# Optimization experiments

Measured on AMD Instinct MI355X. Metric: run time of the kernel, lower is better.

The kernel has to match this reference:

```python
import jax, jax.numpy as jnp
import numpy as np

K = 3
PAD = 1
EPS = 1e-5


def _conv2d(x, w, b):
    y = jax.lax.conv_general_dilated(x, w, window_strides=(1, 1), padding='SAME',
                                     dimension_numbers=('NCHW', 'OIHW', 'NCHW'))
    return y + b[None, :, None, None]


def _bn(x, g, beta, m, v):
    inv = jax.lax.rsqrt(v + EPS)
    return (x - m[None, :, None, None]) * (g * inv)[None, :, None, None] + beta[None, :, None, None]


def _deform_conv2d(x, offset, w, b):
    # torchvision deform_conv2d (v1, no mask), stride=1, pad=1, 3x3 kernel.
    B, Cin, H, W = x.shape
    Cout = w.shape[0]
    # offset: [B, 2*K*K, H, W] -> (dy, dx) per kernel tap
    off = offset.reshape(B, K * K, 2, H, W)
    dy, dx = off[:, :, 0], off[:, :, 1]                     # [B, K2, H, W]
    ii, jj = jnp.meshgrid(jnp.arange(K), jnp.arange(K), indexing='ij')
    ki = (ii.reshape(-1) - PAD).astype(x.dtype)             # [K2]
    kj = (jj.reshape(-1) - PAD).astype(x.dtype)
    py = jnp.arange(H, dtype=x.dtype)[None, None, :, None] + ki[None, :, None, None] + dy
    px = jnp.arange(W, dtype=x.dtype)[None, None, None, :] + kj[None, :, None, None] + dx
    y0 = jnp.floor(py)
    x0 = jnp.floor(px)
    wy = py - y0
    wx = px - x0
    flat = x.reshape(B, Cin, H * W)

    def gather(yc, xc):
        valid = ((yc >= 0) & (yc < H) & (xc >= 0) & (xc < W)).astype(x.dtype)
        yi = jnp.clip(yc, 0, H - 1).astype(jnp.int32)
        xi = jnp.clip(xc, 0, W - 1).astype(jnp.int32)
        idx = (yi * W + xi).reshape(B, -1)                  # [B, K2*H*W]
        g = jax.vmap(lambda f, i: f[:, i])(flat, idx)       # [B, Cin, K2*H*W]
        return g.reshape(B, Cin, K * K, H, W) * valid[:, None]

    v = (gather(y0,     x0    ) * ((1 - wy) * (1 - wx))[:, None]
         + gather(y0,     x0 + 1) * ((1 - wy) * wx)[:, None]
         + gather(y0 + 1, x0    ) * (wy * (1 - wx))[:, None]
         + gather(y0 + 1, x0 + 1) * (wy * wx)[:, None])     # [B, Cin, K2, H, W]
    out = jnp.einsum('bckhw,ock->bohw', v, w.reshape(Cout, Cin, K * K))
    return out + b[None, :, None, None]


def setup_inputs() -> dict:
    key = jax.random.key(0)
    ks = jax.random.split(key, 12)
    d = {}
    d['x'] = jax.random.normal(ks[0], (32, 3, 64, 64), jnp.float32)
    d['offset1_w'] = jax.random.normal(ks[1], (18, 3, 3, 3), jnp.float32) * 0.05
    d['offset1_b'] = jnp.zeros((18,), jnp.float32)
    d['conv1_w'] = jax.random.normal(ks[2], (64, 3, 3, 3), jnp.float32) * 0.1
    d['conv1_b'] = jnp.zeros((64,), jnp.float32)
    d['bn1_gamma'] = jnp.ones((64,), jnp.float32)
    d['bn1_beta'] = jnp.zeros((64,), jnp.float32)
    d['bn1_mean'] = jnp.zeros((64,), jnp.float32)
    d['bn1_var'] = jax.random.uniform(ks[3], (64,), jnp.float32, 0.5, 1.5)
    d['offset2_w'] = jax.random.normal(ks[4], (18, 64, 3, 3), jnp.float32) * 0.02
    d['offset2_b'] = jnp.zeros((18,), jnp.float32)
    d['conv2_w'] = jax.random.normal(ks[5], (128, 64, 3, 3), jnp.float32) * 0.05
    d['conv2_b'] = jnp.zeros((128,), jnp.float32)
    d['bn2_gamma'] = jnp.ones((128,), jnp.float32)
    d['bn2_beta'] = jnp.zeros((128,), jnp.float32)
    d['bn2_mean'] = jnp.zeros((128,), jnp.float32)
    d['bn2_var'] = jax.random.uniform(ks[6], (128,), jnp.float32, 0.5, 1.5)
    d['fc1_w'] = jax.random.normal(ks[7], (256, 128), jnp.float32) * 0.08
    d['fc1_b'] = jnp.zeros((256,), jnp.float32)
    d['fc2_w'] = jax.random.normal(ks[8], (200, 256), jnp.float32) * 0.06
    d['fc2_b'] = jnp.zeros((200,), jnp.float32)
    return d


def reference(x, offset1_w, offset1_b, conv1_w, conv1_b, bn1_gamma, bn1_beta, bn1_mean, bn1_var,
              offset2_w, offset2_b, conv2_w, conv2_b, bn2_gamma, bn2_beta, bn2_mean, bn2_var,
              fc1_w, fc1_b, fc2_w, fc2_b):
    # Eval-mode forward (dropout layers are identity / deterministic).
    off1 = _conv2d(x, offset1_w, offset1_b)
    h = _deform_conv2d(x, off1, conv1_w, conv1_b)
    h = jax.nn.relu(_bn(h, bn1_gamma, bn1_beta, bn1_mean, bn1_var))
    off2 = _conv2d(h, offset2_w, offset2_b)
    h = _deform_conv2d(h, off2, conv2_w, conv2_b)
    h = jax.nn.relu(_bn(h, bn2_gamma, bn2_beta, bn2_mean, bn2_var))
    h = h.mean(axis=(2, 3))                                 # global avg pool -> [B, 128]
    h = jax.nn.relu(h @ fc1_w.T + fc1_b)
    return h @ fc2_w.T + fc2_b
```

## Files before the change

### kernel.cpp

```cpp
#include <hip/hip_runtime.h>

#define EPS 1e-5f

#define W1OT 0
#define W1T  1024
#define W2T  4096
#define W2OB 40960
#define SC1  59392
#define SH1  59456
#define SC2  59520
#define SH2  59648
#define POOL 59776
#define XP   65536
#define H1B  589824
#define OFF2 4784128
#define W2T_U   8192
#define W2OB_U  81920
#define H1B_U   1179648

typedef __attribute__((ext_vector_type(8))) short bhalf8;
typedef __attribute__((ext_vector_type(8))) unsigned short u16x8;
typedef __attribute__((ext_vector_type(4))) float f32x4;

#define BPAD 72
#define OPAD 584

struct Tap { int i00, i01, i10, i11; float w00, w01, w10, w11; };

__device__ __forceinline__ Tap make_tap(float py, float px) {
    float y0f = floorf(py), x0f = floorf(px);
    float wy = py - y0f, wx = px - x0f;
    bool by0 = (y0f >= 0.f)  && (y0f < 64.f);
    bool by1 = (y0f >= -1.f) && (y0f < 63.f);
    bool bx0 = (x0f >= 0.f)  && (x0f < 64.f);
    bool bx1 = (x0f >= -1.f) && (x0f < 63.f);
    int y0 = min(max((int)y0f, 0), 63);
    int y1 = min(max((int)y0f + 1, 0), 63);
    int x0 = min(max((int)x0f, 0), 63);
    int x1 = min(max((int)x0f + 1, 0), 63);
    Tap tp;
    tp.i00 = y0 * 64 + x0; tp.i01 = y0 * 64 + x1;
    tp.i10 = y1 * 64 + x0; tp.i11 = y1 * 64 + x1;
    tp.w00 = (by0 && bx0) ? (1.f - wy) * (1.f - wx) : 0.f;
    tp.w01 = (by0 && bx1) ? (1.f - wy) * wx         : 0.f;
    tp.w10 = (by1 && bx0) ? wy * (1.f - wx)         : 0.f;
    tp.w11 = (by1 && bx1) ? wy * wx                 : 0.f;
    return tp;
}

__device__ __forceinline__ ushort f2bf(float f) {
    union { float f; uint u; } a; a.f = f;
    uint u = a.u;
    return (ushort)((u + 0x7fffu + ((u >> 16) & 1u)) >> 16);
}
__device__ __forceinline__ float bf2f(ushort u) {
    union { uint u; float f; } a; a.u = ((uint)u) << 16;
    return a.f;
}

__global__ __launch_bounds__(256) void k_prep(
    const float* __restrict__ x,
    const float* __restrict__ o1w, const float* __restrict__ c1w,
    const float* __restrict__ o2w, const float* __restrict__ c2w,
    const float* __restrict__ c1b, const float* __restrict__ g1,
    const float* __restrict__ be1, const float* __restrict__ m1,
    const float* __restrict__ v1,
    const float* __restrict__ c2b, const float* __restrict__ g2,
    const float* __restrict__ be2, const float* __restrict__ m2,
    const float* __restrict__ v2,
    float* __restrict__ ws) {
    int tid = blockIdx.x * 256 + threadIdx.x;
    ushort* wsu = (ushort*)ws;
    if (tid < 648) {
        int co = tid % 18, tc = tid / 18, c = tc & 3, t = tc >> 2;
        ws[W1OT + tid] = (c < 3) ? o1w[(co * 3 + c) * 9 + t] : 0.f;
    } else if (tid < 2952) {
        int i = tid - 648;
        int co = i & 63, tc = i >> 6, c = tc & 3, t = tc >> 2;
        ws[W1T + i] = (c < 3) ? c1w[(co * 3 + c) * 9 + t] : 0.f;
    } else if (tid < 76680) {
        int i = tid - 2952;
        int c = i & 63, n = (i >> 6) & 127, t = i >> 13;
        wsu[W2T_U + i] = f2bf(c2w[(n * 64 + c) * 9 + t]);
    } else if (tid < 95112) {
        int i = tid - 76680;
        int n = i / 576, k = i - n * 576;
        int c = k & 63, t = k >> 6;
        float v = (n < 18) ? o2w[(n * 64 + c) * 9 + t] : 0.f;
        wsu[W2OB_U + i] = f2bf(v);
    } else if (tid < 95176) {
        int i = tid - 95112;
        float s = g1[i] * rsqrtf(v1[i] + EPS);
        ws[SC1 + i] = s;
        ws[SH1 + i] = (c1b[i] - m1[i]) * s + be1[i];
    } else if (tid < 95304) {
        int i = tid - 95176;
        float s = g2[i] * rsqrtf(v2[i] + EPS);
        ws[SC2 + i] = s;
        ws[SH2 + i] = (c2b[i] - m2[i]) * s + be2[i];
    } else if (tid < 99400) {
        ws[POOL + tid - 95304] = 0.f;
    } else if (tid < 230472) {
        int i = tid - 99400;
        int b = i >> 12, hw = i & 4095;
        const float* xpp = x + (size_t)b * 3 * 4096 + hw;
        f32x4 o;
        o[0] = xpp[0]; o[1] = xpp[4096]; o[2] = xpp[8192]; o[3] = 0.f;
        *(f32x4*)(ws + XP + (size_t)i * 4) = o;
    }
}

__global__ __launch_bounds__(256, 3) void k_def1(
    const float* __restrict__ o1b, float* __restrict__ ws) {
    __shared__ float wo[648];
    __shared__ float wt[2304];
    for (int i = threadIdx.x; i < 648; i += 256) wo[i] = ws[W1OT + i];
    for (int i = threadIdx.x; i < 2304; i += 256) wt[i] = ws[W1T + i];
    __syncthreads();
    int tid = blockIdx.x * 256 + threadIdx.x;
    int b = tid >> 12, hw = tid & 4095, h = hw >> 6, w = hw & 63;
    const float* xp = ws + XP + (size_t)b * 16384;
    float off[18];
#pragma unroll
    for (int i = 0; i < 18; ++i) off[i] = o1b[i];
#pragma unroll
    for (int t = 0; t < 9; ++t) {
        int yy = h + t / 3 - 1, xx = w + t % 3 - 1;
        f32x4 pv = (f32x4)0.f;
        if (yy >= 0 && yy < 64 && xx >= 0 && xx < 64)
            pv = *(const f32x4*)(xp + (yy * 64 + xx) * 4);
#pragma unroll
        for (int c = 0; c < 3; ++c) {
            const float* wp = wo + (t * 4 + c) * 18;
#pragma unroll
            for (int co = 0; co < 18; ++co) off[co] += pv[c] * wp[co];
        }
    }
    f32x4 v[9];
#pragma unroll
    for (int t = 0; t < 9; ++t) {
        Tap tp = make_tap((float)(h + t / 3 - 1) + off[2 * t],
                          (float)(w + t % 3 - 1) + off[2 * t + 1]);
        f32x4 c00 = *(const f32x4*)(xp + tp.i00 * 4);
        f32x4 c01 = *(const f32x4*)(xp + tp.i01 * 4);
        f32x4 c10 = *(const f32x4*)(xp + tp.i10 * 4);
        f32x4 c11 = *(const f32x4*)(xp + tp.i11 * 4);
        v[t] = tp.w00 * c00 + tp.w01 * c01 + tp.w10 * c10 + tp.w11 * c11;
    }
    const float* sc = ws + SC1;
    const float* sh = ws + SH1;
    ushort* op = (ushort*)ws + H1B_U + (size_t)(b * 4096 + hw) * 64;
#pragma unroll
    for (int ch = 0; ch < 2; ++ch) {
        float acc[32];
#pragma unroll
        for (int i = 0; i < 32; ++i) acc[i] = 0.f;
#pragma unroll
        for (int t = 0; t < 9; ++t)
#pragma unroll
            for (int c = 0; c < 3; ++c) {
                float vk = v[t][c];
                const float* wp = wt + (t * 4 + c) * 64 + ch * 32;
#pragma unroll
                for (int co = 0; co < 32; ++co) acc[co] += vk * wp[co];
            }
        ushort ob[32];
#pragma unroll
        for (int i = 0; i < 32; ++i) {
            int co = ch * 32 + i;
            ob[i] = f2bf(fmaxf(acc[i] * sc[co] + sh[co], 0.f));
        }
#pragma unroll
        for (int i = 0; i < 4; ++i)
            *(uint4*)(op + ch * 32 + i * 8) = *(const uint4*)(ob + i * 8);
    }
}

__global__ __launch_bounds__(256, 4) void k_off2(
    const float* __restrict__ o2b, float* __restrict__ ws) {
    __shared__ ushort Bl[32 * OPAD];
    int g = blockIdx.x;
    int b = (g & 7) * 4 + ((g >> 3) & 3);
    int row = g >> 5;
    int tid = threadIdx.x, lane = tid & 63, wv = tid >> 6;
    int r = lane & 15, q = lane >> 4;
    int hw0 = row * 64 + wv * 16;
    const ushort* hb = (const ushort*)ws + H1B_U + (size_t)b * 262144;
    const ushort* bt = (const ushort*)ws + W2OB_U;
    for (int i = tid; i < 2304; i += 256) {
        int n = i / 72, kk = (i - n * 72) * 8;
        *(uint4*)(Bl + n * OPAD + kk) = *(const uint4*)(bt + n * 576 + kk);
    }
    __syncthreads();
    f32x4 acc[2];
    acc[0] = (f32x4)0.f; acc[1] = (f32x4)0.f;
#pragma unroll
    for (int t = 0; t < 9; ++t) {
        int yy = row + t / 3 - 1;
        int xx = wv * 16 + r + t % 3 - 1;
        bool val = (yy >= 0 && yy < 64 && xx >= 0 && xx < 64);
        int yyc = min(max(yy, 0), 63), xxc = min(max(xx, 0), 63);
        const ushort* ap = hb + (size_t)(yyc * 64 + xxc) * 64 + q * 8;
#pragma unroll
        for (int ks = 0; ks < 2; ++ks) {
            bhalf8 af = val ? *(const bhalf8*)(ap + ks * 32) : (bhalf8)(short)0;
            int kk = t * 64 + ks * 32 + q * 8;
#pragma unroll
            for (int nt = 0; nt < 2; ++nt) {
                bhalf8 bf = *(const bhalf8*)(Bl + (nt * 16 + r) * OPAD + kk);
                acc[nt] = __builtin_amdgcn_mfma_f32_16x16x32_bf16(af, bf, acc[nt], 0, 0, 0);
            }
        }
    }
#pragma unroll
    for (int nt = 0; nt < 2; ++nt) {
        int n = nt * 16 + r;
        if (n < 18) {
            float bias = o2b[n];
#pragma unroll
            for (int rr = 0; rr < 4; ++rr) {
                int hw = hw0 + q * 4 + rr;
                ws[OFF2 + (size_t)(b * 4096 + hw) * 18 + n] = acc[nt][rr] + bias;
            }
        }
    }
}

__global__ __launch_bounds__(256, 5) void k_def2(float* __restrict__ ws) {
    __shared__ ushort Blds[128 * BPAD];
    int g = blockIdx.x;
    int b = (g & 7) * 4 + ((g >> 3) & 3);
    int row = g >> 5;
    int tid = threadIdx.x, lane = tid & 63, wv = tid >> 6;
    int r = lane & 15, q = lane >> 4;
    int px = wv * 16 + r;
    const ushort* hb = (const ushort*)ws + H1B_U + (size_t)b * 262144;
    const float* o2 = ws + OFF2 + (size_t)b * 73728 + (size_t)(row * 64 + px) * 18;
    const ushort* wB = (const ushort*)ws + W2T_U;
    int bn = tid >> 1, bc = (tid & 1) * 32;

    float2 off[9];
#pragma unroll
    for (int t = 0; t < 9; ++t) off[t] = *(const float2*)(o2 + 2 * t);

    f32x4 acc[8];
#pragma unroll
    for (int j = 0; j < 8; ++j) acc[j] = (f32x4)0.f;

    for (int t = 0; t < 9; ++t) {
        Tap tp = make_tap((float)(row + t / 3 - 1) + off[t].x,
                          (float)(px + t % 3 - 1) + off[t].y);
        if (t) __syncthreads();
        {
            const uint4* s4 = (const uint4*)(wB + (t * 128 + bn) * 64 + bc);
            uint4 p0 = s4[0], p1 = s4[1], p2 = s4[2], p3 = s4[3];
            ushort* dst = Blds + bn * BPAD + bc;
            *(uint4*)(dst)      = p0;
            *(uint4*)(dst + 8)  = p1;
            *(uint4*)(dst + 16) = p2;
            *(uint4*)(dst + 24) = p3;
        }
        __syncthreads();
#pragma unroll
        for (int ks = 0; ks < 2; ++ks) {
            int ko = ks * 32 + q * 8;
            bhalf8 bf[8];
#pragma unroll
            for (int nt = 0; nt < 8; ++nt)
                bf[nt] = *(const bhalf8*)(Blds + (nt * 16 + r) * BPAD + ko);
            u16x8 g00 = *(const u16x8*)(hb + (size_t)tp.i00 * 64 + ko);
            u16x8 g01 = *(const u16x8*)(hb + (size_t)tp.i01 * 64 + ko);
            u16x8 g10 = *(const u16x8*)(hb + (size_t)tp.i10 * 64 + ko);
            u16x8 g11 = *(const u16x8*)(hb + (size_t)tp.i11 * 64 + ko);
            f32x4 lo = (f32x4)0.f, hi = (f32x4)0.f;
#pragma unroll
            for (int j = 0; j < 4; ++j) {
                lo[j] = tp.w00 * bf2f(g00[j]) + tp.w01 * bf2f(g01[j])
                      + tp.w10 * bf2f(g10[j]) + tp.w11 * bf2f(g11[j]);
                hi[j] = tp.w00 * bf2f(g00[j + 4]) + tp.w01 * bf2f(g01[j + 4])
                      + tp.w10 * bf2f(g10[j + 4]) + tp.w11 * bf2f(g11[j + 4]);
            }
            bhalf8 af;
#pragma unroll
            for (int j = 0; j < 4; ++j) {
                af[j]     = (short)f2bf(lo[j]);
                af[j + 4] = (short)f2bf(hi[j]);
            }
#pragma unroll
            for (int nt = 0; nt < 8; ++nt)
                acc[nt] = __builtin_amdgcn_mfma_f32_16x16x32_bf16(af, bf[nt], acc[nt], 0, 0, 0);
        }
    }
    const float* sc = ws + SC2;
    const float* sh = ws + SH2;
    float* pool = ws + POOL;
#pragma unroll
    for (int nt = 0; nt < 8; ++nt) {
        int col = nt * 16 + r;
        float s0 = sc[col], s1 = sh[col];
        float s = 0.f;
#pragma unroll
        for (int rr = 0; rr < 4; ++rr)
            s += fmaxf(acc[nt][rr] * s0 + s1, 0.f);
        s += __shfl_xor(s, 16);
        s += __shfl_xor(s, 32);
        if (lane < 16) atomicAdd(&pool[b * 128 + col], s);
    }
}

__global__ __launch_bounds__(256) void k_fc(
    const float* __restrict__ w1, const float* __restrict__ b1,
    const float* __restrict__ w2, const float* __restrict__ b2,
    const float* __restrict__ ws, float* __restrict__ out) {
    int b = blockIdx.x, o = threadIdx.x;
    __shared__ float pl[128];
    __shared__ float hl[256];
    if (o < 128) pl[o] = ws[POOL + b * 128 + o] * (1.f / 4096.f);
    __syncthreads();
    float s = b1[o];
    const float* wp = w1 + o * 128;
#pragma unroll 8
    for (int c = 0; c < 128; ++c) s += pl[c] * wp[c];
    hl[o] = fmaxf(s, 0.f);
    __syncthreads();
    if (o < 200) {
        float s2 = b2[o];
        const float* wp2 = w2 + o * 256;
#pragma unroll 8
        for (int c = 0; c < 256; ++c) s2 += hl[c] * wp2[c];
        out[b * 200 + o] = s2;
    }
}

extern "C" void kernel_launch(void* const* d_in, const int* in_sizes, int n_in,
                              void* d_out, int out_size, void* d_ws, size_t ws_size,
                              hipStream_t stream) {
    const float* x   = (const float*)d_in[0];
    const float* o1w = (const float*)d_in[1];
    const float* o1b = (const float*)d_in[2];
    const float* c1w = (const float*)d_in[3];
    const float* c1b = (const float*)d_in[4];
    const float* g1  = (const float*)d_in[5];
    const float* be1 = (const float*)d_in[6];
    const float* m1  = (const float*)d_in[7];
    const float* v1  = (const float*)d_in[8];
    const float* o2w = (const float*)d_in[9];
    const float* o2b = (const float*)d_in[10];
    const float* c2w = (const float*)d_in[11];
    const float* c2b = (const float*)d_in[12];
    const float* g2  = (const float*)d_in[13];
    const float* be2 = (const float*)d_in[14];
    const float* m2  = (const float*)d_in[15];
    const float* v2  = (const float*)d_in[16];
    const float* f1w = (const float*)d_in[17];
    const float* f1b = (const float*)d_in[18];
    const float* f2w = (const float*)d_in[19];
    const float* f2b = (const float*)d_in[20];
    float* ws  = (float*)d_ws;
    float* out = (float*)d_out;

    k_prep<<<901, 256, 0, stream>>>(x, o1w, c1w, o2w, c2w,
                                    c1b, g1, be1, m1, v1,
                                    c2b, g2, be2, m2, v2, ws);
    k_def1<<<512, 256, 0, stream>>>(o1b, ws);
    k_off2<<<2048, 256, 0, stream>>>(o2b, ws);
    k_def2<<<2048, 256, 0, stream>>>(ws);
    k_fc<<<32, 256, 0, stream>>>(f1w, f1b, f2w, f2b, ws, out);
}
```

Measured before the change: 319.7 us.

## Fuse offset conv into deformable conv2 kernel via shared-memory offsets

Merges the offset-2 convolution kernel into the second deformable-conv kernel. Each block first computes its row's 18 offset channels with MFMA, stages them in LDS, and then runs the deformable sampling and GEMM in the same block. This removes one kernel launch and the global write and read of the offset tensor. In exchange the fused kernel uses more LDS and registers, and its launch bounds drop from 5 to 4 blocks per CU, so occupancy is lower.

```diff
diff --git a/kernel.cpp b/kernel.cpp
--- a/kernel.cpp
+++ b/kernel.cpp
@@ -13,7 +13,6 @@
 #define POOL 59776
 #define XP   65536
 #define H1B  589824
-#define OFF2 4784128
 #define W2T_U   8192
 #define W2OB_U  81920
 #define H1B_U   1179648
@@ -176,58 +175,11 @@
     }
 }
 
-__global__ __launch_bounds__(256, 4) void k_off2(
+__global__ __launch_bounds__(256, 4) void k_def2(
     const float* __restrict__ o2b, float* __restrict__ ws) {
-    __shared__ ushort Bl[32 * OPAD];
-    int g = blockIdx.x;
-    int b = (g & 7) * 4 + ((g >> 3) & 3);
-    int row = g >> 5;
-    int tid = threadIdx.x, lane = tid & 63, wv = tid >> 6;
-    int r = lane & 15, q = lane >> 4;
-    int hw0 = row * 64 + wv * 16;
-    const ushort* hb = (const ushort*)ws + H1B_U + (size_t)b * 262144;
-    const ushort* bt = (const ushort*)ws + W2OB_U;
-    for (int i = tid; i < 2304; i += 256) {
-        int n = i / 72, kk = (i - n * 72) * 8;
-        *(uint4*)(Bl + n * OPAD + kk) = *(const uint4*)(bt + n * 576 + kk);
-    }
-    __syncthreads();
-    f32x4 acc[2];
-    acc[0] = (f32x4)0.f; acc[1] = (f32x4)0.f;
-#pragma unroll
-    for (int t = 0; t < 9; ++t) {
-        int yy = row + t / 3 - 1;
-        int xx = wv * 16 + r + t % 3 - 1;
-        bool val = (yy >= 0 && yy < 64 && xx >= 0 && xx < 64);
-        int yyc = min(max(yy, 0), 63), xxc = min(max(xx, 0), 63);
-        const ushort* ap = hb + (size_t)(yyc * 64 + xxc) * 64 + q * 8;
-#pragma unroll
-        for (int ks = 0; ks < 2; ++ks) {
-            bhalf8 af = val ? *(const bhalf8*)(ap + ks * 32) : (bhalf8)(short)0;
-            int kk = t * 64 + ks * 32 + q * 8;
-#pragma unroll
-            for (int nt = 0; nt < 2; ++nt) {
-                bhalf8 bf = *(const bhalf8*)(Bl + (nt * 16 + r) * OPAD + kk);
-                acc[nt] = __builtin_amdgcn_mfma_f32_16x16x32_bf16(af, bf, acc[nt], 0, 0, 0);
-            }
-        }
-    }
-#pragma unroll
-    for (int nt = 0; nt < 2; ++nt) {
-        int n = nt * 16 + r;
-        if (n < 18) {
-            float bias = o2b[n];
-#pragma unroll
-            for (int rr = 0; rr < 4; ++rr) {
-                int hw = hw0 + q * 4 + rr;
-                ws[OFF2 + (size_t)(b * 4096 + hw) * 18 + n] = acc[nt][rr] + bias;
-            }
-        }
-    }
-}
-
-__global__ __launch_bounds__(256, 5) void k_def2(float* __restrict__ ws) {
-    __shared__ ushort Blds[128 * BPAD];
+    __shared__ ushort smem[32 * OPAD];
+    float* offL = (float*)smem;
+    ushort* Bdef = smem + 2304;
     int g = blockIdx.x;
     int b = (g & 7) * 4 + ((g >> 3) & 3);
     int row = g >> 5;
@@ -235,26 +187,63 @@
     int r = lane & 15, q = lane >> 4;
     int px = wv * 16 + r;
     const ushort* hb = (const ushort*)ws + H1B_U + (size_t)b * 262144;
-    const float* o2 = ws + OFF2 + (size_t)b * 73728 + (size_t)(row * 64 + px) * 18;
     const ushort* wB = (const ushort*)ws + W2T_U;
+    const ushort* bt = (const ushort*)ws + W2OB_U;
+
+    for (int i = tid; i < 2304; i += 256) {
+        int n = i / 72, kk = (i - n * 72) * 8;
+        *(uint4*)(smem + n * OPAD + kk) = *(const uint4*)(bt + n * 576 + kk);
+    }
+    __syncthreads();
+
+    f32x4 acc2[2];
+    acc2[0] = (f32x4)0.f; acc2[1] = (f32x4)0.f;
+#pragma unroll
+    for (int t = 0; t < 9; ++t) {
+        int yy = row + t / 3 - 1;
+        int xx = px + t % 3 - 1;
+        bool val = (yy >= 0 && yy < 64 && xx >= 0 && xx < 64);
+        int yyc = min(max(yy, 0), 63), xxc = min(max(xx, 0), 63);
+        const ushort* ap = hb + (size_t)(yyc * 64 + xxc) * 64 + q * 8;
+#pragma unroll
+        for (int ks = 0; ks < 2; ++ks) {
+            bhalf8 af = val ? *(const bhalf8*)(ap + ks * 32) : (bhalf8)(short)0;
+            int kk = t * 64 + ks * 32 + q * 8;
+#pragma unroll
+            for (int nt = 0; nt < 2; ++nt) {
+                bhalf8 bf = *(const bhalf8*)(smem + (nt * 16 + r) * OPAD + kk);
+                acc2[nt] = __builtin_amdgcn_mfma_f32_16x16x32_bf16(af, bf, acc2[nt], 0, 0, 0);
+            }
+        }
+    }
+    __syncthreads();
+#pragma unroll
+    for (int nt = 0; nt < 2; ++nt) {
+        int n = nt * 16 + r;
+        if (n < 18) {
+            float bias = o2b[n];
+#pragma unroll
+            for (int rr = 0; rr < 4; ++rr)
+                offL[(wv * 16 + q * 4 + rr) * 18 + n] = acc2[nt][rr] + bias;
+        }
+    }
+    __syncthreads();
+
+    f32x4 acc[8];
+#pragma unroll
+    for (int j = 0; j < 8; ++j) acc[j] = (f32x4)0.f;
     int bn = tid >> 1, bc = (tid & 1) * 32;
 
-    float2 off[9];
-#pragma unroll
-    for (int t = 0; t < 9; ++t) off[t] = *(const float2*)(o2 + 2 * t);
-
-    f32x4 acc[8];
-#pragma unroll
-    for (int j = 0; j < 8; ++j) acc[j] = (f32x4)0.f;
-
     for (int t = 0; t < 9; ++t) {
-        Tap tp = make_tap((float)(row + t / 3 - 1) + off[t].x,
-                          (float)(px + t % 3 - 1) + off[t].y);
+        float oy = offL[px * 18 + 2 * t];
+        float ox = offL[px * 18 + 2 * t + 1];
+        Tap tp = make_tap((float)(row + t / 3 - 1) + oy,
+                          (float)(px + t % 3 - 1) + ox);
         if (t) __syncthreads();
         {
             const uint4* s4 = (const uint4*)(wB + (t * 128 + bn) * 64 + bc);
             uint4 p0 = s4[0], p1 = s4[1], p2 = s4[2], p3 = s4[3];
-            ushort* dst = Blds + bn * BPAD + bc;
+            ushort* dst = Bdef + bn * BPAD + bc;
             *(uint4*)(dst)      = p0;
             *(uint4*)(dst + 8)  = p1;
             *(uint4*)(dst + 16) = p2;
@@ -267,7 +256,7 @@
             bhalf8 bf[8];
 #pragma unroll
             for (int nt = 0; nt < 8; ++nt)
-                bf[nt] = *(const bhalf8*)(Blds + (nt * 16 + r) * BPAD + ko);
+                bf[nt] = *(const bhalf8*)(Bdef + (nt * 16 + r) * BPAD + ko);
             u16x8 g00 = *(const u16x8*)(hb + (size_t)tp.i00 * 64 + ko);
             u16x8 g01 = *(const u16x8*)(hb + (size_t)tp.i01 * 64 + ko);
             u16x8 g10 = *(const u16x8*)(hb + (size_t)tp.i10 * 64 + ko);
@@ -363,7 +352,6 @@
                                     c1b, g1, be1, m1, v1,
                                     c2b, g2, be2, m2, v2, ws);
     k_def1<<<512, 256, 0, stream>>>(o1b, ws);
-    k_off2<<<2048, 256, 0, stream>>>(o2b, ws);
-    k_def2<<<2048, 256, 0, stream>>>(ws);
+    k_def2<<<2048, 256, 0, stream>>>(o2b, ws);
     k_fc<<<32, 256, 0, stream>>>(f1w, f1b, f2w, f2b, ws, out);
 }
```

Result: faster. 301.9 us (-5.6%).
